# Optimization experiments

Measured on AMD Instinct MI355X. Metric: run time of the kernel, lower is better.

Reference implementation:

```python
import jax, jax.numpy as jnp
import numpy as np

N, E, F_IN = 50000, 800000, 128
H1, C1 = 4, 32          # layer 1: heads, channels (concat -> 128)
H2, C2 = 1, 40          # layer 2: out heads, num_class (mean over heads)
NEG_SLOPE = 0.2


def setup_inputs() -> dict:
    key = jax.random.key(0)
    ks = jax.random.split(key, 10)
    x = jax.random.normal(ks[0], (N, F_IN), dtype=jnp.float32)
    edge_index = jax.random.randint(ks[1], (2, E), 0, N, dtype=jnp.int32)
    s1 = 1.0 / np.sqrt(F_IN)
    s2 = 1.0 / np.sqrt(H1 * C1)
    W1 = jax.random.normal(ks[2], (F_IN, H1 * C1), dtype=jnp.float32) * s1
    att_src1 = jax.random.normal(ks[3], (H1, C1), dtype=jnp.float32) * s1
    att_dst1 = jax.random.normal(ks[4], (H1, C1), dtype=jnp.float32) * s1
    b1 = jnp.zeros((H1 * C1,), dtype=jnp.float32)
    W2 = jax.random.normal(ks[5], (H1 * C1, H2 * C2), dtype=jnp.float32) * s2
    att_src2 = jax.random.normal(ks[6], (H2, C2), dtype=jnp.float32) * s2
    att_dst2 = jax.random.normal(ks[7], (H2, C2), dtype=jnp.float32) * s2
    b2 = jnp.zeros((C2,), dtype=jnp.float32)
    return {"x": x, "edge_index": edge_index, "W1": W1, "att_src1": att_src1,
            "att_dst1": att_dst1, "b1": b1, "W2": W2, "att_src2": att_src2,
            "att_dst2": att_dst2, "b2": b2}


def _gat_layer(x, src, dst, W, a_src, a_dst, b, concat):
    # PyG GATConv (eval): linear -> per-head attention logits on edges ->
    # segment-softmax over each destination's in-edges -> scatter-aggregate.
    n = x.shape[0]
    Hh, C = a_src.shape
    h = (x @ W).reshape(n, Hh, C)                       # [N,H,C]
    al_s = jnp.sum(h * a_src, axis=-1)                  # [N,H]
    al_d = jnp.sum(h * a_dst, axis=-1)                  # [N,H]
    alpha = jax.nn.leaky_relu(al_s[src] + al_d[dst], NEG_SLOPE)  # [E,H]
    m = jax.lax.stop_gradient(jax.ops.segment_max(alpha, dst, num_segments=n))
    e = jnp.exp(alpha - m[dst])
    denom = jax.ops.segment_sum(e, dst, num_segments=n)
    a = e / (denom[dst] + 1e-16)                        # [E,H]
    out = jax.ops.segment_sum(h[src] * a[..., None], dst, num_segments=n)
    out = out.reshape(n, Hh * C) if concat else out.mean(axis=1)
    return out + b


def reference(x, edge_index, W1, att_src1, att_dst1, b1, W2, att_src2, att_dst2, b2):
    n = x.shape[0]
    loop = jnp.arange(n, dtype=edge_index.dtype)        # GATConv add_self_loops=True
    src = jnp.concatenate([edge_index[0], loop])
    dst = jnp.concatenate([edge_index[1], loop])
    h = _gat_layer(x, src, dst, W1, att_src1, att_dst1, b1, concat=True)
    h = jax.nn.elu(h)
    out = _gat_layer(h, src, dst, W2, att_src2, att_dst2, b2, concat=False)
    return out
```

## Files before the change

### kernel.cpp

```cpp
#include <hip/hip_runtime.h>
#include <hip/hip_bf16.h>
#include <hip/hip_fp16.h>
#include <math.h>

constexpr int N_NODES = 50000;
constexpr int E_EDGES = 800000;
constexpr float NEG_SLOPE = 0.2f;
constexpr int CAP = 64;
constexpr int G1_BLOCKS   = (N_NODES + 63) / 64;
constexpr int LINK_BLOCKS = (E_EDGES + 255) / 256;

typedef _Float16 half8 __attribute__((ext_vector_type(8)));
typedef _Float16 half2v __attribute__((ext_vector_type(2)));
typedef float    floatx4 __attribute__((ext_vector_type(4)));

static inline int cdiv(long long a, int b) { return (int)((a + b - 1) / b); }

__device__ inline float leaky(float a) { return a > 0.f ? a : NEG_SLOPE * a; }
__device__ inline unsigned pack2h(float a, float b) {
    union { _Float16 h[2]; unsigned u; } p;
    p.h[0] = (_Float16)a; p.h[1] = (_Float16)b; return p.u;
}
__device__ inline float2 unp2h(unsigned u) {
    __half2 hh = *reinterpret_cast<__half2*>(&u);
    return __half22float2(hh);
}
__device__ inline float sel4(const float4& v, int h) {
    float a = (h & 2) ? v.z : v.x;
    float b = (h & 2) ? v.w : v.y;
    return (h & 1) ? b : a;
}

__global__ __launch_bounds__(256) void prep_kernel(const float* __restrict__ W1,
                                                   const float* __restrict__ W2,
                                                   int* __restrict__ deg,
                                                   _Float16* __restrict__ w1t,
                                                   _Float16* __restrict__ w2t) {
    int b = blockIdx.x, t = threadIdx.x;
    if (b < 196) {
        int i = b * 256 + t;
        if (i < N_NODES) deg[i] = 0;
        return;
    }
    if (b < 196 + 64) {
        int idx = (b - 196) * 256 + t;
        int k = idx >> 7, c = idx & 127;
        w1t[c * 128 + k] = (_Float16)W1[k * 128 + c];
        return;
    }
    {
        int idx = (b - 260) * 256 + t;
        int k = idx / 40, c = idx - k * 40;
        w2t[c * 128 + k] = (_Float16)W2[k * 40 + c];
    }
}

__global__ __launch_bounds__(256, 8) void gemm1_link_kernel(const float* __restrict__ x,
                                                            const _Float16* __restrict__ w1t,
                                                            const float* __restrict__ as1,
                                                            const float* __restrict__ ad1,
                                                            unsigned short* __restrict__ h1h,
                                                            float* __restrict__ als,
                                                            float* __restrict__ ald,
                                                            const int* __restrict__ ei,
                                                            int* __restrict__ deg,
                                                            unsigned short* __restrict__ csr16) {
    __shared__ _Float16 xS[64 * 136];
    __shared__ float asld[128], adld[128];
    int t = threadIdx.x;

    if (blockIdx.x >= G1_BLOCKS) {
        int e = (blockIdx.x - G1_BLOCKS) * 256 + t;
        if (e < E_EDGES) {
            int s = ei[e], d = ei[E_EDGES + e];
            int slot = atomicAdd(&deg[d], 1) + 1;
            if (slot < CAP) csr16[d * CAP + slot] = (unsigned short)s;
        }
        return;
    }

    int row0 = blockIdx.x * 64;
    if (t < 128) { asld[t] = as1[t]; adld[t] = ad1[t]; }
    #pragma unroll
    for (int i = 0; i < 8; ++i) {
        int fi = i * 256 + t;
        int r = fi >> 5, c4 = (fi & 31) * 4;
        int gr = row0 + r;
        float4 v = make_float4(0.f, 0.f, 0.f, 0.f);
        if (gr < N_NODES) v = *(const float4*)&x[(size_t)gr * 128 + c4];
        union { _Float16 h[4]; uint2 u; } pk;
        pk.h[0] = (_Float16)v.x; pk.h[1] = (_Float16)v.y;
        pk.h[2] = (_Float16)v.z; pk.h[3] = (_Float16)v.w;
        *(uint2*)&xS[r * 136 + c4] = pk.u;
    }
    __syncthreads();

    int w = t >> 6, lane = t & 63, quad = lane >> 4, l16 = lane & 15;
    floatx4 z = {0.f, 0.f, 0.f, 0.f};
    floatx4 c[4][2];
    #pragma unroll
    for (int rt = 0; rt < 4; ++rt) { c[rt][0] = z; c[rt][1] = z; }

    const _Float16* wt0 = w1t + (size_t)(w * 32 + l16) * 128;
    const _Float16* wt1 = wt0 + 16 * 128;
    #pragma unroll
    for (int ks = 0; ks < 4; ++ks) {
        int kg = ks * 32 + quad * 8;
        half8 b0 = *(const half8*)&wt0[kg];
        half8 b1 = *(const half8*)&wt1[kg];
        #pragma unroll
        for (int rt = 0; rt < 4; ++rt) {
            half8 a = *(const half8*)&xS[(rt * 16 + l16) * 136 + kg];
            c[rt][0] = __builtin_amdgcn_mfma_f32_16x16x32_f16(a, b0, c[rt][0], 0, 0, 0);
            c[rt][1] = __builtin_amdgcn_mfma_f32_16x16x32_f16(a, b1, c[rt][1], 0, 0, 0);
        }
    }
    __syncthreads();
    _Float16* cbuf = xS;
    #pragma unroll
    for (int rt = 0; rt < 4; ++rt)
        #pragma unroll
        for (int ctl = 0; ctl < 2; ++ctl)
            #pragma unroll
            for (int reg = 0; reg < 4; ++reg)
                cbuf[(rt * 16 + quad * 4 + reg) * 136 + (w * 32 + ctl * 16 + l16)]
                    = (_Float16)c[rt][ctl][reg];
    __syncthreads();
    int r = t >> 2, hq = t & 3;
    int n = row0 + r;
    if (n < N_NODES) {
        if (hq == 0) csr16[n * CAP] = (unsigned short)n;
        float ps = 0.f, pd = 0.f;
        #pragma unroll
        for (int i = 0; i < 4; ++i) {
            uint4 uv = *(uint4*)&cbuf[r * 136 + hq * 32 + i * 8];
            *(uint4*)&h1h[(size_t)n * 128 + hq * 32 + i * 8] = uv;
            union { uint4 u; _Float16 h[8]; } cv; cv.u = uv;
            #pragma unroll
            for (int k = 0; k < 8; ++k) {
                float v = (float)cv.h[k];
                ps += v * asld[hq * 32 + i * 8 + k];
                pd += v * adld[hq * 32 + i * 8 + k];
            }
        }
        als[n * 4 + hq] = ps;
        ald[n * 4 + hq] = pd;
    }
}

__global__ __launch_bounds__(256) void agg1_kernel(const int* __restrict__ deg_,
                                                   const unsigned short* __restrict__ csr16,
                                                   const float* __restrict__ als,
                                                   const float4* __restrict__ ald4,
                                                   const unsigned short* __restrict__ h1h,
                                                   const float* __restrict__ b1,
                                                   unsigned short* __restrict__ out1h) {
    int wv   = threadIdx.x >> 6;
    int lane = threadIdx.x & 63;
    int half = lane >> 5;
    int l    = lane & 31;
    int myhead = l >> 3;
    int we   = lane & 15;
    int wh   = lane >> 4;
    int d    = blockIdx.x * 4 + wv;
    int dg   = min(deg_[d] + 1, CAP);
    int base = d * CAP;
    float4 aldd = ald4[d];
    float d_hw = sel4(aldd, wh);

    float sm = 0.f;
    float acc[4] = {0.f, 0.f, 0.f, 0.f};
    int sfirst = (int)csr16[base];
    #pragma unroll 2
    for (int j = 0; j < dg; j += 16) {
        int s_w = (int)csr16[base + j + we];
        float av = als[s_w * 4 + wh];
        float wgt = (j + we < dg) ? __expf(leaky(av + d_hw)) : 0.f;
        uint4 blkA = *(const uint4*)&csr16[base + j];
        uint4 blkB = *(const uint4*)&csr16[base + j + 8];
        unsigned bw[8] = { blkA.x, blkA.y, blkA.z, blkA.w,
                           blkB.x, blkB.y, blkB.z, blkB.w };
        int ss[8];
        #pragma unroll
        for (int p = 0; p < 8; ++p) {
            unsigned b = __builtin_amdgcn_readfirstlane(bw[p]);
            int e0 = (int)(b & 0xffff), e1 = (int)(b >> 16);
            int mys = half ? e1 : e0;
            if (j + 2 * p + half >= dg) mys = sfirst;
            ss[p] = mys;
        }
        uint2 hv[8];
        #pragma unroll
        for (int p = 0; p < 8; ++p)
            hv[p] = *(const uint2*)(h1h + ((size_t)ss[p] << 7) + 4 * l);
        float ww[8];
        #pragma unroll
        for (int p = 0; p < 8; ++p) {
            ww[p] = __shfl(wgt, 16 * myhead + 2 * p + half);
            sm += ww[p];
        }
        half2v hacc0 = { (_Float16)0.f, (_Float16)0.f };
        half2v hacc1 = { (_Float16)0.f, (_Float16)0.f };
        #pragma unroll
        for (int p = 0; p < 8; ++p) {
            half2v v0 = *reinterpret_cast<half2v*>(&hv[p].x);
            half2v v1 = *reinterpret_cast<half2v*>(&hv[p].y);
            _Float16 hw = (_Float16)ww[p];
            half2v hwv = { hw, hw };
            hacc0 += v0 * hwv;
            hacc1 += v1 * hwv;
        }
        acc[0] += (float)hacc0[0]; acc[1] += (float)hacc0[1];
        acc[2] += (float)hacc1[0]; acc[3] += (float)hacc1[1];
    }
    sm += __shfl_xor(sm, 32);
    #pragma unroll
    for (int k = 0; k < 4; ++k) acc[k] += __shfl_xor(acc[k], 32);
    if (half == 0) {
        float inv = 1.f / (sm + 1e-16f);
        float v[4];
        #pragma unroll
        for (int k = 0; k < 4; ++k) {
            v[k] = acc[k] * inv + b1[4 * l + k];
            v[k] = v[k] > 0.f ? v[k] : __expf(v[k]) - 1.f;
        }
        uint2 o;
        o.x = pack2h(v[0], v[1]);
        o.y = pack2h(v[2], v[3]);
        *(uint2*)&out1h[(size_t)d * 128 + 4 * l] = o;
    }
}

__global__ __launch_bounds__(256, 8) void gemm2_kernel(const unsigned short* __restrict__ out1h,
                                                       const _Float16* __restrict__ w2t,
                                                       const float* __restrict__ as2,
                                                       const float* __restrict__ ad2,
                                                       unsigned short* __restrict__ h2h,
                                                       float* __restrict__ als,
                                                       float* __restrict__ ald) {
    __shared__ _Float16 aS[64 * 136];
    __shared__ float asld[40], adld[40];
    int t = threadIdx.x;
    int row0 = blockIdx.x * 64;
    if (t < 40) { asld[t] = as2[t]; adld[t] = ad2[t]; }
    #pragma unroll
    for (int i = 0; i < 4; ++i) {
        int fi = i * 256 + t;
        int r = fi >> 4, s8 = (fi & 15) * 8;
        int gr = row0 + r;
        uint4 v = make_uint4(0u, 0u, 0u, 0u);
        if (gr < N_NODES) v = *(const uint4*)&out1h[(size_t)gr * 128 + s8];
        *(uint4*)&aS[r * 136 + s8] = v;
    }
    __syncthreads();

    int w = t >> 6, lane = t & 63, quad = lane >> 4, l16 = lane & 15;
    floatx4 z = {0.f, 0.f, 0.f, 0.f};
    floatx4 c0 = z, c1 = z, c2 = z;
    int n2 = (l16 < 8) ? 32 + l16 : 39;
    const _Float16* wb0 = w2t + (size_t)l16 * 128;
    const _Float16* wb1 = w2t + (size_t)(16 + l16) * 128;
    const _Float16* wb2 = w2t + (size_t)n2 * 128;
    #pragma unroll
    for (int ks = 0; ks < 4; ++ks) {
        int kg = ks * 32 + quad * 8;
        half8 b0 = *(const half8*)&wb0[kg];
        half8 b1 = *(const half8*)&wb1[kg];
        half8 b2 = *(const half8*)&wb2[kg];
        half8 a  = *(const half8*)&aS[(w * 16 + l16) * 136 + kg];
        c0 = __builtin_amdgcn_mfma_f32_16x16x32_f16(a, b0, c0, 0, 0, 0);
        c1 = __builtin_amdgcn_mfma_f32_16x16x32_f16(a, b1, c1, 0, 0, 0);
        c2 = __builtin_amdgcn_mfma_f32_16x16x32_f16(a, b2, c2, 0, 0, 0);
    }
    __syncthreads();
    #pragma unroll
    for (int reg = 0; reg < 4; ++reg) {
        int rr = (w * 16 + quad * 4 + reg) * 136;
        aS[rr + l16]      = (_Float16)c0[reg];
        aS[rr + 16 + l16] = (_Float16)c1[reg];
        aS[rr + 32 + l16] = (_Float16)c2[reg];
    }
    __syncthreads();
    for (int fi = t; fi < 320; fi += 256) {
        int r = fi / 5, s = fi - r * 5;
        int n = row0 + r;
        if (n < N_NODES) {
            uint4 v = *(uint4*)&aS[r * 136 + s * 8];
            *(uint4*)&h2h[(size_t)n * 40 + s * 8] = v;
        }
    }
    int r = t >> 2, q = t & 3;
    int n = row0 + r;
    float ps = 0.f, pd = 0.f;
    #pragma unroll
    for (int i = 0; i < 10; ++i) {
        int cc = q * 10 + i;
        float v = (float)aS[r * 136 + cc];
        ps += v * asld[cc]; pd += v * adld[cc];
    }
    ps += __shfl_xor(ps, 1); ps += __shfl_xor(ps, 2);
    pd += __shfl_xor(pd, 1); pd += __shfl_xor(pd, 2);
    if (q == 0 && n < N_NODES) { als[n] = ps; ald[n] = pd; }
}

__global__ __launch_bounds__(256) void agg2_kernel(const int* __restrict__ deg_,
                                                   const unsigned short* __restrict__ csr16,
                                                   const float* __restrict__ als,
                                                   const float* __restrict__ ald,
                                                   const unsigned short* __restrict__ h2h,
                                                   const float* __restrict__ b2,
                                                   float* __restrict__ out) {
    int wv   = threadIdx.x >> 6;
    int lane = threadIdx.x & 63;
    int d    = blockIdx.x * 4 + wv;
    int dg   = min(deg_[d] + 1, CAP);
    int base = d * CAP;
    float aldd = ald[d];

    int slot = lane / 20;
    int idx  = lane - slot * 20;
    int sfirst = (int)csr16[base];
    float sm = 0.f, acc0 = 0.f, acc1 = 0.f;
    if (lane < 60) {
        for (int jb = 0; jb < dg; jb += 12) {
            int ss[4]; unsigned hv[4]; float ww[4];
            #pragma unroll
            for (int i = 0; i < 4; ++i) {
                int jj = jb + slot + 3 * i;
                ss[i] = (jj < dg) ? (int)csr16[base + jj] : sfirst;
            }
            #pragma unroll
            for (int i = 0; i < 4; ++i)
                hv[i] = *(const unsigned*)(h2h + (size_t)ss[i] * 40 + 2 * idx);
            #pragma unroll
            for (int i = 0; i < 4; ++i) {
                int jj = jb + slot + 3 * i;
                float w = __expf(leaky(als[ss[i]] + aldd));
                ww[i] = (jj < dg) ? w : 0.f;
            }
            #pragma unroll
            for (int i = 0; i < 4; ++i) {
                float2 f = unp2h(hv[i]);
                acc0 += f.x * ww[i]; acc1 += f.y * ww[i]; sm += ww[i];
            }
        }
    }
    float s1 = __shfl(sm,   idx + 20), s2 = __shfl(sm,   idx + 40);
    float t0 = __shfl(acc0, idx + 20), t1 = __shfl(acc0, idx + 40);
    float u0 = __shfl(acc1, idx + 20), u1 = __shfl(acc1, idx + 40);
    sm += s1 + s2; acc0 += t0 + t1; acc1 += u0 + u1;
    if (lane < 20) {
        float inv = 1.f / (sm + 1e-16f);
        float2 o = make_float2(acc0 * inv + b2[2 * lane], acc1 * inv + b2[2 * lane + 1]);
        *(float2*)&out[(size_t)d * 40 + 2 * lane] = o;
    }
}

constexpr size_t OFF_H1H    = 0;
constexpr size_t OFF_OUT1   = 3200000;
constexpr size_t OFF_ALS1   = 6400000;
constexpr size_t OFF_ALD1   = 6600000;
constexpr size_t OFF_W1T    = 6800000;
constexpr size_t OFF_W2T    = 6808192;
constexpr size_t OFF_DEG    = 6860000;
constexpr size_t OFF_CSRF   = 6920000;
constexpr size_t WS_FLOATS  = 10120000;

extern "C" void kernel_launch(void* const* d_in, const int* in_sizes, int n_in,
                              void* d_out, int out_size, void* d_ws, size_t ws_size,
                              hipStream_t stream) {
    const float* x   = (const float*)d_in[0];
    const int*   ei  = (const int*)  d_in[1];
    const float* W1  = (const float*)d_in[2];
    const float* as1 = (const float*)d_in[3];
    const float* ad1 = (const float*)d_in[4];
    const float* b1  = (const float*)d_in[5];
    const float* W2  = (const float*)d_in[6];
    const float* as2 = (const float*)d_in[7];
    const float* ad2 = (const float*)d_in[8];
    const float* b2  = (const float*)d_in[9];
    float* out = (float*)d_out;

    if (ws_size < WS_FLOATS * sizeof(float)) return;

    float* ws = (float*)d_ws;
    unsigned short* h1h   = (unsigned short*)(ws + OFF_H1H);
    unsigned short* h2h   = (unsigned short*)(ws + OFF_H1H);
    unsigned short* out1h = (unsigned short*)(ws + OFF_OUT1);
    float* als1    = ws + OFF_ALS1;
    float* ald1    = ws + OFF_ALD1;
    float* als2    = ws + OFF_ALS1;
    float* ald2    = ws + OFF_ALD1;
    _Float16* w1t  = (_Float16*)(ws + OFF_W1T);
    _Float16* w2t  = (_Float16*)(ws + OFF_W2T);
    int*   deg     = (int*)(ws + OFF_DEG);
    unsigned short* csr16 = (unsigned short*)(ws + OFF_CSRF);

    prep_kernel<<<280, 256, 0, stream>>>(W1, W2, deg, w1t, w2t);
    gemm1_link_kernel<<<G1_BLOCKS + LINK_BLOCKS, 256, 0, stream>>>(
        x, w1t, as1, ad1, h1h, als1, ald1, ei, deg, csr16);

    agg1_kernel<<<N_NODES / 4, 256, 0, stream>>>(deg, csr16, als1,
                                                 (const float4*)ald1,
                                                 h1h, b1, out1h);

    gemm2_kernel<<<cdiv(N_NODES, 64), 256, 0, stream>>>(out1h, w2t, as2, ad2, h2h, als2, ald2);
    agg2_kernel<<<N_NODES / 4, 256, 0, stream>>>(deg, csr16, als2, ald2, h2h, b2, out);
}
```

Baseline: 206.7 us.

## Fuse layer-2 linear projection into layer-1 aggregation kernel

The separate gemm2 kernel is removed. Each wave in agg1 now writes its ELU'd node row to shared memory and computes the 40 layer-2 outputs with per-lane fdot2 dot products against the transposed W2, plus the attention logits through a wave shuffle reduction. This drops the out1h round trip through global memory and one kernel launch, at the cost of scalar dot-product work in place of MFMA and 24 idle lanes per wave during that phase. It also reorders the gemm1/link block indexing so the edge-linking blocks come first, and moves h2h and als2/ald2 to their own workspace buffers so they no longer alias layer-1 data.

```diff
diff --git a/kernel.cpp b/kernel.cpp
--- a/kernel.cpp
+++ b/kernel.cpp
@@ -30,6 +30,16 @@
     float b = (h & 2) ? v.w : v.y;
     return (h & 1) ? b : a;
 }
+
+#if __has_builtin(__builtin_amdgcn_fdot2)
+__device__ inline float dot2f(half2v a, half2v b, float c) {
+    return __builtin_amdgcn_fdot2(a, b, c, false);
+}
+#else
+__device__ inline float dot2f(half2v a, half2v b, float c) {
+    return c + (float)a[0] * (float)b[0] + (float)a[1] * (float)b[1];
+}
+#endif
 
 __global__ __launch_bounds__(256) void prep_kernel(const float* __restrict__ W1,
                                                    const float* __restrict__ W2,
@@ -69,8 +79,8 @@
     __shared__ float asld[128], adld[128];
     int t = threadIdx.x;
 
-    if (blockIdx.x >= G1_BLOCKS) {
-        int e = (blockIdx.x - G1_BLOCKS) * 256 + t;
+    if (blockIdx.x < LINK_BLOCKS) {
+        int e = blockIdx.x * 256 + t;
         if (e < E_EDGES) {
             int s = ei[e], d = ei[E_EDGES + e];
             int slot = atomicAdd(&deg[d], 1) + 1;
@@ -79,7 +89,7 @@
         return;
     }
 
-    int row0 = blockIdx.x * 64;
+    int row0 = (blockIdx.x - LINK_BLOCKS) * 64;
     if (t < 128) { asld[t] = as1[t]; adld[t] = ad1[t]; }
     #pragma unroll
     for (int i = 0; i < 8; ++i) {
@@ -154,7 +164,13 @@
                                                    const float4* __restrict__ ald4,
                                                    const unsigned short* __restrict__ h1h,
                                                    const float* __restrict__ b1,
-                                                   unsigned short* __restrict__ out1h) {
+                                                   const _Float16* __restrict__ w2t,
+                                                   const float* __restrict__ as2g,
+                                                   const float* __restrict__ ad2g,
+                                                   unsigned short* __restrict__ h2h,
+                                                   float* __restrict__ als2,
+                                                   float* __restrict__ ald2) {
+    __shared__ _Float16 rowS[4][128];
     int wv   = threadIdx.x >> 6;
     int lane = threadIdx.x & 63;
     int half = lane >> 5;
@@ -227,80 +243,35 @@
         uint2 o;
         o.x = pack2h(v[0], v[1]);
         o.y = pack2h(v[2], v[3]);
-        *(uint2*)&out1h[(size_t)d * 128 + 4 * l] = o;
-    }
-}
-
-__global__ __launch_bounds__(256, 8) void gemm2_kernel(const unsigned short* __restrict__ out1h,
-                                                       const _Float16* __restrict__ w2t,
-                                                       const float* __restrict__ as2,
-                                                       const float* __restrict__ ad2,
-                                                       unsigned short* __restrict__ h2h,
-                                                       float* __restrict__ als,
-                                                       float* __restrict__ ald) {
-    __shared__ _Float16 aS[64 * 136];
-    __shared__ float asld[40], adld[40];
-    int t = threadIdx.x;
-    int row0 = blockIdx.x * 64;
-    if (t < 40) { asld[t] = as2[t]; adld[t] = ad2[t]; }
-    #pragma unroll
-    for (int i = 0; i < 4; ++i) {
-        int fi = i * 256 + t;
-        int r = fi >> 4, s8 = (fi & 15) * 8;
-        int gr = row0 + r;
-        uint4 v = make_uint4(0u, 0u, 0u, 0u);
-        if (gr < N_NODES) v = *(const uint4*)&out1h[(size_t)gr * 128 + s8];
-        *(uint4*)&aS[r * 136 + s8] = v;
-    }
-    __syncthreads();
-
-    int w = t >> 6, lane = t & 63, quad = lane >> 4, l16 = lane & 15;
-    floatx4 z = {0.f, 0.f, 0.f, 0.f};
-    floatx4 c0 = z, c1 = z, c2 = z;
-    int n2 = (l16 < 8) ? 32 + l16 : 39;
-    const _Float16* wb0 = w2t + (size_t)l16 * 128;
-    const _Float16* wb1 = w2t + (size_t)(16 + l16) * 128;
-    const _Float16* wb2 = w2t + (size_t)n2 * 128;
-    #pragma unroll
-    for (int ks = 0; ks < 4; ++ks) {
-        int kg = ks * 32 + quad * 8;
-        half8 b0 = *(const half8*)&wb0[kg];
-        half8 b1 = *(const half8*)&wb1[kg];
-        half8 b2 = *(const half8*)&wb2[kg];
-        half8 a  = *(const half8*)&aS[(w * 16 + l16) * 136 + kg];
-        c0 = __builtin_amdgcn_mfma_f32_16x16x32_f16(a, b0, c0, 0, 0, 0);
-        c1 = __builtin_amdgcn_mfma_f32_16x16x32_f16(a, b1, c1, 0, 0, 0);
-        c2 = __builtin_amdgcn_mfma_f32_16x16x32_f16(a, b2, c2, 0, 0, 0);
-    }
-    __syncthreads();
-    #pragma unroll
-    for (int reg = 0; reg < 4; ++reg) {
-        int rr = (w * 16 + quad * 4 + reg) * 136;
-        aS[rr + l16]      = (_Float16)c0[reg];
-        aS[rr + 16 + l16] = (_Float16)c1[reg];
-        aS[rr + 32 + l16] = (_Float16)c2[reg];
-    }
-    __syncthreads();
-    for (int fi = t; fi < 320; fi += 256) {
-        int r = fi / 5, s = fi - r * 5;
-        int n = row0 + r;
-        if (n < N_NODES) {
-            uint4 v = *(uint4*)&aS[r * 136 + s * 8];
-            *(uint4*)&h2h[(size_t)n * 40 + s * 8] = v;
-        }
-    }
-    int r = t >> 2, q = t & 3;
-    int n = row0 + r;
-    float ps = 0.f, pd = 0.f;
-    #pragma unroll
-    for (int i = 0; i < 10; ++i) {
-        int cc = q * 10 + i;
-        float v = (float)aS[r * 136 + cc];
-        ps += v * asld[cc]; pd += v * adld[cc];
-    }
-    ps += __shfl_xor(ps, 1); ps += __shfl_xor(ps, 2);
-    pd += __shfl_xor(pd, 1); pd += __shfl_xor(pd, 2);
-    if (q == 0 && n < N_NODES) { als[n] = ps; ald[n] = pd; }
+        *(uint2*)&rowS[wv][4 * l] = o;
+    }
+    float h2c = 0.f;
+    if (lane < 40) {
+        const half8* wr = (const half8*)(w2t + (size_t)lane * 128);
+        const half8* xr = (const half8*)rowS[wv];
+        #pragma unroll
+        for (int kk = 0; kk < 16; ++kk) {
+            half8 a = xr[kk], b = wr[kk];
+            #pragma unroll
+            for (int q = 0; q < 4; ++q) {
+                half2v a2 = { a[2 * q], a[2 * q + 1] };
+                half2v b2 = { b[2 * q], b[2 * q + 1] };
+                h2c = dot2f(a2, b2, h2c);
+            }
+        }
+    }
+    float ps = (lane < 40) ? h2c * as2g[lane] : 0.f;
+    float pd = (lane < 40) ? h2c * ad2g[lane] : 0.f;
+    #pragma unroll
+    for (int off = 1; off < 64; off <<= 1) {
+        ps += __shfl_xor(ps, off);
+        pd += __shfl_xor(pd, off);
+    }
+    if (lane == 0) { als2[d] = ps; ald2[d] = pd; }
+    if (lane < 40) {
+        union { _Float16 h; unsigned short u; } cv; cv.h = (_Float16)h2c;
+        h2h[(size_t)d * 40 + lane] = cv.u;
+    }
 }
 
 __global__ __launch_bounds__(256) void agg2_kernel(const int* __restrict__ deg_,
@@ -357,13 +328,15 @@
 }
 
 constexpr size_t OFF_H1H    = 0;
-constexpr size_t OFF_OUT1   = 3200000;
+constexpr size_t OFF_H2H    = 3200000;
 constexpr size_t OFF_ALS1   = 6400000;
 constexpr size_t OFF_ALD1   = 6600000;
 constexpr size_t OFF_W1T    = 6800000;
 constexpr size_t OFF_W2T    = 6808192;
 constexpr size_t OFF_DEG    = 6860000;
 constexpr size_t OFF_CSRF   = 6920000;
+constexpr size_t OFF_ALS2   = 8520000;
+constexpr size_t OFF_ALD2   = 8570000;
 constexpr size_t WS_FLOATS  = 10120000;
 
 extern "C" void kernel_launch(void* const* d_in, const int* in_sizes, int n_in,
@@ -385,12 +358,11 @@
 
     float* ws = (float*)d_ws;
     unsigned short* h1h   = (unsigned short*)(ws + OFF_H1H);
-    unsigned short* h2h   = (unsigned short*)(ws + OFF_H1H);
-    unsigned short* out1h = (unsigned short*)(ws + OFF_OUT1);
+    unsigned short* h2h   = (unsigned short*)(ws + OFF_H2H);
     float* als1    = ws + OFF_ALS1;
     float* ald1    = ws + OFF_ALD1;
-    float* als2    = ws + OFF_ALS1;
-    float* ald2    = ws + OFF_ALD1;
+    float* als2    = ws + OFF_ALS2;
+    float* ald2    = ws + OFF_ALD2;
     _Float16* w1t  = (_Float16*)(ws + OFF_W1T);
     _Float16* w2t  = (_Float16*)(ws + OFF_W2T);
     int*   deg     = (int*)(ws + OFF_DEG);
@@ -402,8 +374,8 @@
 
     agg1_kernel<<<N_NODES / 4, 256, 0, stream>>>(deg, csr16, als1,
                                                  (const float4*)ald1,
-                                                 h1h, b1, out1h);
-
-    gemm2_kernel<<<cdiv(N_NODES, 64), 256, 0, stream>>>(out1h, w2t, as2, ad2, h2h, als2, ald2);
+                                                 h1h, b1, w2t, as2, ad2,
+                                                 h2h, als2, ald2);
+
     agg2_kernel<<<N_NODES / 4, 256, 0, stream>>>(deg, csr16, als2, ald2, h2h, b2, out);
 }
```

Measured after the change: 267.3 us. 1.29x slower.

## Stage W1 tiles in shared memory and launch edge-link blocks first

Applied to the files above, without the earlier changes.

The layer-1 GEMM now copies the transposed fp16 W1 into a padded shared-memory tile in two K-chunks, so B operands are read from LDS instead of strided global loads. That tile is then reused as the output staging buffer. The block order puts the CSR edge-linking blocks before the GEMM blocks so the atomic-heavy work starts earlier, and the occupancy hint in launch bounds is removed. The layer-2 aggregation loop also gets an unroll-by-2 hint. Shared memory per block roughly doubles, which may lower occupancy, and extra barriers are added.

```diff
diff --git a/kernel.cpp b/kernel.cpp
--- a/kernel.cpp
+++ b/kernel.cpp
@@ -55,22 +55,23 @@
     }
 }
 
-__global__ __launch_bounds__(256, 8) void gemm1_link_kernel(const float* __restrict__ x,
-                                                            const _Float16* __restrict__ w1t,
-                                                            const float* __restrict__ as1,
-                                                            const float* __restrict__ ad1,
-                                                            unsigned short* __restrict__ h1h,
-                                                            float* __restrict__ als,
-                                                            float* __restrict__ ald,
-                                                            const int* __restrict__ ei,
-                                                            int* __restrict__ deg,
-                                                            unsigned short* __restrict__ csr16) {
+__global__ __launch_bounds__(256) void gemm1_link_kernel(const float* __restrict__ x,
+                                                         const _Float16* __restrict__ w1t,
+                                                         const float* __restrict__ as1,
+                                                         const float* __restrict__ ad1,
+                                                         unsigned short* __restrict__ h1h,
+                                                         float* __restrict__ als,
+                                                         float* __restrict__ ald,
+                                                         const int* __restrict__ ei,
+                                                         int* __restrict__ deg,
+                                                         unsigned short* __restrict__ csr16) {
     __shared__ _Float16 xS[64 * 136];
+    __shared__ _Float16 wtS[128 * 72];
     __shared__ float asld[128], adld[128];
     int t = threadIdx.x;
 
-    if (blockIdx.x >= G1_BLOCKS) {
-        int e = (blockIdx.x - G1_BLOCKS) * 256 + t;
+    if (blockIdx.x < LINK_BLOCKS) {
+        int e = blockIdx.x * 256 + t;
         if (e < E_EDGES) {
             int s = ei[e], d = ei[E_EDGES + e];
             int slot = atomicAdd(&deg[d], 1) + 1;
@@ -79,7 +80,7 @@
         return;
     }
 
-    int row0 = blockIdx.x * 64;
+    int row0 = (blockIdx.x - LINK_BLOCKS) * 64;
     if (t < 128) { asld[t] = as1[t]; adld[t] = ad1[t]; }
     #pragma unroll
     for (int i = 0; i < 8; ++i) {
@@ -93,7 +94,6 @@
         pk.h[2] = (_Float16)v.z; pk.h[3] = (_Float16)v.w;
         *(uint2*)&xS[r * 136 + c4] = pk.u;
     }
-    __syncthreads();
 
     int w = t >> 6, lane = t & 63, quad = lane >> 4, l16 = lane & 15;
     floatx4 z = {0.f, 0.f, 0.f, 0.f};
@@ -101,22 +101,31 @@
     #pragma unroll
     for (int rt = 0; rt < 4; ++rt) { c[rt][0] = z; c[rt][1] = z; }
 
-    const _Float16* wt0 = w1t + (size_t)(w * 32 + l16) * 128;
-    const _Float16* wt1 = wt0 + 16 * 128;
-    #pragma unroll
-    for (int ks = 0; ks < 4; ++ks) {
-        int kg = ks * 32 + quad * 8;
-        half8 b0 = *(const half8*)&wt0[kg];
-        half8 b1 = *(const half8*)&wt1[kg];
-        #pragma unroll
-        for (int rt = 0; rt < 4; ++rt) {
-            half8 a = *(const half8*)&xS[(rt * 16 + l16) * 136 + kg];
-            c[rt][0] = __builtin_amdgcn_mfma_f32_16x16x32_f16(a, b0, c[rt][0], 0, 0, 0);
-            c[rt][1] = __builtin_amdgcn_mfma_f32_16x16x32_f16(a, b1, c[rt][1], 0, 0, 0);
+    #pragma unroll
+    for (int kc = 0; kc < 2; ++kc) {
+        __syncthreads();
+        #pragma unroll
+        for (int i = 0; i < 4; ++i) {
+            int fi = i * 256 + t;
+            int col = fi >> 3, k8 = (fi & 7) * 8;
+            *(uint4*)&wtS[col * 72 + k8] = *(const uint4*)&w1t[col * 128 + kc * 64 + k8];
+        }
+        __syncthreads();
+        #pragma unroll
+        for (int ks2 = 0; ks2 < 2; ++ks2) {
+            int ko = ks2 * 32 + quad * 8;
+            half8 b0 = *(const half8*)&wtS[(w * 32 + l16) * 72 + ko];
+            half8 b1 = *(const half8*)&wtS[(w * 32 + 16 + l16) * 72 + ko];
+            #pragma unroll
+            for (int rt = 0; rt < 4; ++rt) {
+                half8 a = *(const half8*)&xS[(rt * 16 + l16) * 136 + kc * 64 + ko];
+                c[rt][0] = __builtin_amdgcn_mfma_f32_16x16x32_f16(a, b0, c[rt][0], 0, 0, 0);
+                c[rt][1] = __builtin_amdgcn_mfma_f32_16x16x32_f16(a, b1, c[rt][1], 0, 0, 0);
+            }
         }
     }
     __syncthreads();
-    _Float16* cbuf = xS;
+    _Float16* cbuf = wtS;
     #pragma unroll
     for (int rt = 0; rt < 4; ++rt)
         #pragma unroll
@@ -322,6 +331,7 @@
     int sfirst = (int)csr16[base];
     float sm = 0.f, acc0 = 0.f, acc1 = 0.f;
     if (lane < 60) {
+        #pragma unroll 2
         for (int jb = 0; jb < dg; jb += 12) {
             int ss[4]; unsigned hv[4]; float ww[4];
             #pragma unroll
```

Result: slower. 224.7 us (+8.7%).
